# Optimization experiments

Hardware: AMD Instinct MI355X
Metric: run time of the kernel (lower is better)

## Reference

```python
import jax, jax.numpy as jnp
import numpy as np

TAPS, DIMS, SPS = 32, 2, 2
LR_W, LR_F, LR_S, LR_B = 1.0 / 2**6, 1.0 / 2**7, 0.0, 1.0 / 2**11
GRAD_MAX_W, GRAD_MAX_F = 30.0, 30.0
EPS, BETA = 1e-8, 0.0


def _const16qam():
    # commplax comm.const('16QAM', norm=True): unit-average-power 16QAM grid
    p = np.array([-3.0, -1.0, 1.0, 3.0], dtype=np.float32)
    c = (p[:, None] + 1j * p[None, :]).reshape(-1) / np.sqrt(10.0)
    return jnp.asarray(c, dtype=jnp.complex64)


def _frame(x, flen, fstep):
    # xop.frame: [L, D] -> [(L-flen)//fstep + 1, flen, D]
    n = (x.shape[0] - flen) // fstep + 1
    idx = jnp.arange(n)[:, None] * fstep + jnp.arange(flen)[None, :]
    return x[idx]


def _clip(g, gmax):
    # same math as jnp.where(|g|>gmax, g/|g|*gmax, g), but NaN-safe under AD
    ag = jnp.abs(g)
    return g * jnp.minimum(1.0, gmax / jnp.maximum(ag, 1e-30))


def _ddlms(x):
    const = _const16qam()
    u_all = _frame(x, TAPS, SPS)  # [N, taps, dims] complex64

    def step(state, u):
        w, f, s, b, fshat = state
        v = jnp.einsum('ijt,tj->i', w, u)          # mimo filter output [dims]
        k = v * f
        c = k * s
        z = c + b
        q = v * fshat + b
        # decision-directed symbol (train=False, no truth)
        d = const[jnp.argmin(jnp.abs(const[:, None] - q[None, :]), axis=0)]
        psi_hat = jnp.abs(f) / f * jnp.abs(s) / s
        e_w = (d - b) * psi_hat - v
        e_f = d - b - k
        e_s = d - b - c
        e_b = d - z
        gw = -1.0 / ((jnp.abs(u) ** 2).sum() + EPS) * e_w[:, None, None] * u.conj().T[None, ...]
        gf = -1.0 / (jnp.abs(v) ** 2 + EPS) * e_f * v.conj()
        gs = -1.0 / (jnp.abs(k) ** 2 + EPS) * e_s * k.conj()
        gb = -e_b
        gw = _clip(gw, GRAD_MAX_W)
        gf = _clip(gf, GRAD_MAX_F)
        out = (w, f, s, b)  # pre-update params are used by apply
        wn = w - LR_W * gw
        fn = f - LR_F * gf
        sn = s - LR_S * gs
        bn = b - LR_B * gb
        fshatn = BETA * fshat + (1.0 - BETA) * (fn * sn)
        return (wn, fn, sn, bn, fshatn), out

    dt = jnp.complex64
    state0 = (jnp.zeros((DIMS, DIMS, TAPS), dt),   # w0 (mimoinit='zeros')
              jnp.ones((DIMS,), dt),               # f0
              jnp.ones((DIMS,), dt),               # s0
              jnp.zeros((DIMS,), dt),              # b0
              jnp.ones((DIMS,), dt))               # fshat0
    _, (ws, fs, ss, bs) = jax.lax.scan(step, state0, u_all)
    # mimo_apply: vmap(mimo)(ws, u_all) * fs * ss + bs
    y = jnp.einsum('nijt,ntj->ni', ws, u_all) * fs * ss + bs  # [N, dims]
    return y


def setup_inputs() -> dict:
    key = jax.random.key(0)
    k1, k2 = jax.random.split(key)
    x_re = jax.random.normal(k1, (200000, 2), dtype=jnp.float32)
    x_im = jax.random.normal(k2, (200000, 2), dtype=jnp.float32)
    return {"x_re": x_re, "x_im": x_im}


def reference(x_re, x_im):
    x = jax.lax.complex(x_re, x_im)  # [2N, 2] complex64
    y = _ddlms(x)                    # [(2N-taps)//sps + 1, 2] complex64
    return jnp.stack([y.real, y.imag], axis=-1)  # [N_out, 2, 2] float32
```

## Files before the change

### kernel.cpp

```cpp
#include <hip/hip_runtime.h>

typedef unsigned u2v __attribute__((ext_vector_type(2)));

template<int CTRL>
__device__ __forceinline__ float dpp_xadd(float v) {
    int s = __builtin_amdgcn_update_dpp(0, __float_as_int(v), CTRL, 0xF, 0xF, true);
    return v + __int_as_float(s);
}

#if __has_builtin(__builtin_amdgcn_permlane16_swap)
__device__ __forceinline__ float xor16_add(float v) {
    u2v r = __builtin_amdgcn_permlane16_swap((unsigned)__float_as_int(v),
                                             (unsigned)__float_as_int(v),
                                             false, false);
    return __int_as_float((int)r.x) + __int_as_float((int)r.y);
}
#else
__device__ __forceinline__ float xor16_add(float v) {
    int s = __builtin_amdgcn_ds_swizzle(__float_as_int(v), 0x401F);
    return v + __int_as_float(s);
}
#endif

__device__ __forceinline__ float red32(float v) {
    v = dpp_xadd<0xB1>(v);
    v = dpp_xadd<0x4E>(v);
    v = dpp_xadd<0x141>(v);
    v = dpp_xadd<0x140>(v);
    v = xor16_add(v);
    return v;
}

__global__ void pre_tab(const float* __restrict__ xre,
                        const float* __restrict__ xim,
                        float4* __restrict__ tab, int ns) {
    int n = blockIdx.x * blockDim.x + threadIdx.x;
    if (n >= ns) return;
    const float* ar = xre + 4 * n;
    const float* ai = xim + 4 * n;
    float un = 0.f;
    #pragma unroll 8
    for (int k = 0; k < 64; ++k) un = fmaf(ar[k], ar[k], fmaf(ai[k], ai[k], un));
    float s = (1.0f / 64.0f) / (un + 1e-8f);
    float cr = 0.f, ci = 0.f;
    if (n + 1 < ns) {
        const float* br_ = ar + 4;
        const float* bi_ = ai + 4;
        #pragma unroll 8
        for (int k = 0; k < 64; ++k) {
            cr = fmaf(ar[k], br_[k], fmaf(ai[k], bi_[k], cr));
            ci = fmaf(ar[k], bi_[k], ci);
            ci = fmaf(-ai[k], br_[k], ci);
        }
    }
    tab[n] = make_float4(s, s * cr, s * ci, 0.f);
}

template<bool PRE>
__global__ __launch_bounds__(64, 1)
void ddlms_scan(const float* __restrict__ xre,
                const float* __restrict__ xim,
                const float4* __restrict__ tab,
                float* __restrict__ out) {
    const int l = (int)threadIdx.x;
    const int m = l & 31;
    const int half = l >> 5;

    constexpr float EPSv = 1e-8f;
    constexpr float LRW  = 1.0f / 64.0f;
    constexpr float LRF  = 1.0f / 128.0f;
    constexpr float LRB  = 1.0f / 2048.0f;
    const float B1 = 0.6324555320336759f;
    const float A1 = 0.31622776601683794f;
    const float A3 = 0.9486832980505138f;

    float wAr=0.f, wAi=0.f, wBr=0.f, wBi=0.f;
    float fr=1.f, fi=0.f, br=0.f, bi=0.f;
    float psr=1.f, psj=0.f;
    float vr=0.f, vi=0.f;
    float ewPr=0.f, ewPi=0.f, sP=0.f;

    float2* __restrict__ o2 = reinterpret_cast<float2*>(out);
    const int NS = 99985;

    auto LOADU = [&](int nn, float& a, float& b_, float& c, float& d_) {
        const float* pr = xre + 4 * nn;
        const float* pi = xim + 4 * nn;
        a = pr[m]; c = pr[m + 32]; b_ = pi[m]; d_ = pi[m + 32];
    };

    float pAr, pAi, pBr, pBi;
    float qAr, qAi, qBr, qBi;
    float rAr, rAi, rBr, rBi;
    pAr = pAi = pBr = pBi = 0.f;
    LOADU(0, qAr, qAi, qBr, qBi);
    LOADU(1, rAr, rAi, rBr, rBi);

    auto STEP = [&](int n,
        float& uPAr, float& uPAi, float& uPBr, float& uPBi,
        float& uCAr, float& uCAi, float& uCBr, float& uCBi,
        float& uNAr, float& uNAi, float& uNBr, float& uNBi) {

        {
            float gr = ewPr * uPAr; gr = fmaf( ewPi, uPAi, gr);
            float gi = ewPi * uPAr; gi = fmaf(-ewPr, uPAi, gi);
            wAr = fmaf(sP, gr, wAr); wAi = fmaf(sP, gi, wAi);
            float hr = ewPr * uPBr; hr = fmaf( ewPi, uPBi, hr);
            float hi = ewPi * uPBr; hi = fmaf(-ewPr, uPBi, hi);
            wBr = fmaf(sP, hr, wBr); wBi = fmaf(sP, hi, wBi);
        }

        float basr, basi;
        {
            float prr = wAr * uNAr; prr = fmaf(-wAi, uNAi, prr);
            prr = fmaf(wBr, uNBr, prr); prr = fmaf(-wBi, uNBi, prr);
            float pri = wAr * uNAi; pri = fmaf( wAi, uNAr, pri);
            pri = fmaf(wBr, uNBi, pri); pri = fmaf( wBi, uNBr, pri);
            basr = red32(prr); basi = red32(pri);
        }

        float sN, sCr, sCi;
        if constexpr (PRE) {
            float4 t = tab[n];
            sN = t.x; sCr = t.y; sCi = t.z;
        } else {
            float uu = uCAr * uCAr; uu = fmaf(uCAi, uCAi, uu);
            uu = fmaf(uCBr, uCBr, uu); uu = fmaf(uCBi, uCBi, uu);
            sN = LRW * __builtin_amdgcn_rcpf(red32(uu) + EPSv);
            float ccr = uCAr * uNAr; ccr = fmaf(uCAi, uNAi, ccr);
            ccr = fmaf(uCBr, uNBr, ccr); ccr = fmaf(uCBi, uNBi, ccr);
            float cci = uCAr * uNAi; cci = fmaf(-uCAi, uNAr, cci);
            cci = fmaf(uCBr, uNBi, cci); cci = fmaf(-uCBi, uNBr, cci);
            sCr = sN * red32(ccr); sCi = sN * red32(cci);
        }

        float kr = fmaf(vr, fr, -(vi * fi));
        float ki = fmaf(vr, fi,   vi * fr);
        float zr = kr + br, zi = ki + bi;
        if (m == 0) o2[2 * n + half] = make_float2(zr, zi);

        float magr = (fabsf(zr) > B1) ? A3 : A1;
        float dr   = (zr <= 0.f) ? -magr : magr;
        float magi = (fabsf(zi) > B1) ? A3 : A1;
        float di   = (zi <= 0.f) ? -magi : magi;

        float er = dr - zr, ei = di - zi;

        float v2  = fmaf(vr, vr, fmaf(vi, vi, EPSv));
        float rv  = __builtin_amdgcn_rcpf(v2);
        float gfr = fmaf(er, vr,   ei * vi)  * rv;
        float gfi = fmaf(ei, vr, -(er * vi)) * rv;
        float m2  = fmaf(gfr, gfr, gfi * gfi);
        float scf = fminf(1.f, 30.f * __builtin_amdgcn_rsqf(m2));
        float tf  = LRF * scf;

        float dbr = dr - br, dbi = di - bi;
        float ewr = fmaf(dbr, psr, -(dbi * psj)) - vr;
        float ewi = fmaf(dbr, psj,   dbi * psr)  - vi;

        float Dr = fmaf(ewr, sCr, -(ewi * sCi));
        float Di = fmaf(ewr, sCi,   ewi * sCr);
        vr = basr + Dr;
        vi = basi + Di;

        fr = fmaf(tf, gfr, fr); fi = fmaf(tf, gfi, fi);
        br = fmaf(LRB, er, br); bi = fmaf(LRB, ei, bi);

        float ff = fmaf(fr, fr, fi * fi);
        float rs = __builtin_amdgcn_rsqf(ff);
        psr = fr * rs; psj = -(fi * rs);

        ewPr = ewr; ewPi = ewi; sP = sN;

        int nn = n + 2; if (nn > NS - 1) nn = NS - 1;
        LOADU(nn, uPAr, uPAi, uPBr, uPBi);
    };

    int n = 0;
    for (int it = 0; it < 33328; ++it) {
        STEP(n,     pAr,pAi,pBr,pBi,  qAr,qAi,qBr,qBi,  rAr,rAi,rBr,rBi);
        STEP(n + 1, qAr,qAi,qBr,qBi,  rAr,rAi,rBr,rBi,  pAr,pAi,pBr,pBi);
        STEP(n + 2, rAr,rAi,rBr,rBi,  pAr,pAi,pBr,pBi,  qAr,qAi,qBr,qBi);
        n += 3;
    }
    STEP(99984, pAr,pAi,pBr,pBi, qAr,qAi,qBr,qBi, rAr,rAi,rBr,rBi);
}

extern "C" void kernel_launch(void* const* d_in, const int* in_sizes, int n_in,
                              void* d_out, int out_size, void* d_ws, size_t ws_size,
                              hipStream_t stream) {
    const float* xre = (const float*)d_in[0];
    const float* xim = (const float*)d_in[1];
    float* out = (float*)d_out;
    const int NS = 99985;

    if (ws_size >= (size_t)NS * sizeof(float4)) {
        float4* tab = (float4*)d_ws;
        pre_tab<<<(NS + 255) / 256, 256, 0, stream>>>(xre, xim, tab, NS);
        ddlms_scan<true><<<1, 64, 0, stream>>>(xre, xim, tab, out);
    } else {
        ddlms_scan<false><<<1, 64, 0, stream>>>(xre, xim, nullptr, out);
    }
}
```

Before: 23.38 ms.

## Use packed f32 complex math and deepen input/table prefetch to three steps

Rewrites the serial DD-LMS scan's complex arithmetic with inline-asm packed v_pk_mul/v_pk_fma helpers operating on float2 pairs, cutting VALU instruction count on the per-step critical path. The input ring buffer grows from three to four slots and the precomputed table entry is now prefetched three steps ahead instead of loaded in the step that uses it, hiding global memory latency. The table layout is reordered so the scale and correlation terms load as packed pairs. Hand-written asm limits compiler scheduling, and packed ops may not shorten the dependent latency chain.

```diff
diff --git a/kernel.cpp b/kernel.cpp
--- a/kernel.cpp
+++ b/kernel.cpp
@@ -1,5 +1,6 @@
 #include <hip/hip_runtime.h>
 
+typedef float f2 __attribute__((ext_vector_type(2)));
 typedef unsigned u2v __attribute__((ext_vector_type(2)));
 
 template<int CTRL>
@@ -29,6 +30,57 @@
     v = dpp_xadd<0x140>(v);
     v = xor16_add(v);
     return v;
+}
+
+
+__device__ __forceinline__ f2 cmul(f2 a, f2 b) {
+    f2 t, r;
+    asm("v_pk_mul_f32 %0, %1, %2 op_sel_hi:[0,1]" : "=v"(t) : "v"(a), "v"(b));
+    asm("v_pk_fma_f32 %0, %1, %2, %3 op_sel:[1,1,0] op_sel_hi:[1,0,1] neg_lo:[1,0,0]"
+        : "=v"(r) : "v"(a), "v"(b), "v"(t));
+    return r;
+}
+
+__device__ __forceinline__ f2 cmulc(f2 a, f2 b) {
+    f2 t, r;
+    asm("v_pk_mul_f32 %0, %1, %2 op_sel_hi:[1,0]" : "=v"(t) : "v"(a), "v"(b));
+    asm("v_pk_fma_f32 %0, %1, %2, %3 op_sel:[1,1,0] op_sel_hi:[0,1,1] neg_hi:[1,0,0]"
+        : "=v"(r) : "v"(a), "v"(b), "v"(t));
+    return r;
+}
+
+__device__ __forceinline__ f2 cfma(f2 a, f2 b, f2 acc) {
+    f2 t, r;
+    asm("v_pk_fma_f32 %0, %1, %2, %3 op_sel_hi:[0,1,1]"
+        : "=v"(t) : "v"(a), "v"(b), "v"(acc));
+    asm("v_pk_fma_f32 %0, %1, %2, %3 op_sel:[1,1,0] op_sel_hi:[1,0,1] neg_lo:[1,0,0]"
+        : "=v"(r) : "v"(a), "v"(b), "v"(t));
+    return r;
+}
+
+__device__ __forceinline__ f2 cadd(f2 a, f2 b) {
+    f2 r; asm("v_pk_add_f32 %0, %1, %2" : "=v"(r) : "v"(a), "v"(b)); return r;
+}
+__device__ __forceinline__ f2 csub(f2 a, f2 b) {
+    f2 r;
+    asm("v_pk_add_f32 %0, %1, %2 neg_lo:[0,1] neg_hi:[0,1]" : "=v"(r) : "v"(a), "v"(b));
+    return r;
+}
+__device__ __forceinline__ f2 smul(f2 s, f2 a) {
+    f2 r;
+    asm("v_pk_mul_f32 %0, %1, %2 op_sel_hi:[0,1]" : "=v"(r) : "v"(s), "v"(a));
+    return r;
+}
+__device__ __forceinline__ f2 smulconj(f2 s, f2 a) {
+    f2 r;
+    asm("v_pk_mul_f32 %0, %1, %2 op_sel_hi:[0,1] neg_hi:[0,1]" : "=v"(r) : "v"(s), "v"(a));
+    return r;
+}
+__device__ __forceinline__ f2 sfma(f2 s, f2 g, f2 w) {
+    f2 r;
+    asm("v_pk_fma_f32 %0, %1, %2, %3 op_sel_hi:[0,1,1]"
+        : "=v"(r) : "v"(s), "v"(g), "v"(w));
+    return r;
 }
 
 __global__ void pre_tab(const float* __restrict__ xre,
@@ -53,7 +105,7 @@
             ci = fmaf(-ai[k], br_[k], ci);
         }
     }
-    tab[n] = make_float4(s, s * cr, s * ci, 0.f);
+    tab[n] = make_float4(s, 0.f, s * cr, s * ci);
 }
 
 template<bool PRE>
@@ -74,116 +126,117 @@
     const float A1 = 0.31622776601683794f;
     const float A3 = 0.9486832980505138f;
 
-    float wAr=0.f, wAi=0.f, wBr=0.f, wBi=0.f;
-    float fr=1.f, fi=0.f, br=0.f, bi=0.f;
-    float psr=1.f, psj=0.f;
-    float vr=0.f, vi=0.f;
-    float ewPr=0.f, ewPi=0.f, sP=0.f;
+    f2 wA = {0.f, 0.f}, wB = {0.f, 0.f};
+    f2 ff2 = {1.f, 0.f};
+    f2 bb  = {0.f, 0.f};
+    f2 psi = {1.f, 0.f};
+    f2 vv  = {0.f, 0.f};
+    f2 ewP = {0.f, 0.f};
+    f2 sPv = {0.f, 0.f};
+    const f2 LRBD = {LRB, LRB};
 
     float2* __restrict__ o2 = reinterpret_cast<float2*>(out);
     const int NS = 99985;
 
-    auto LOADU = [&](int nn, float& a, float& b_, float& c, float& d_) {
+    auto LOADU = [&](int nn, f2& a, f2& b_) {
         const float* pr = xre + 4 * nn;
         const float* pi = xim + 4 * nn;
-        a = pr[m]; c = pr[m + 32]; b_ = pi[m]; d_ = pi[m + 32];
+        a.x = pr[m];      a.y = pi[m];
+        b_.x = pr[m + 32]; b_.y = pi[m + 32];
     };
-
-    float pAr, pAi, pBr, pBi;
-    float qAr, qAi, qBr, qBi;
-    float rAr, rAi, rBr, rBi;
-    pAr = pAi = pBr = pBi = 0.f;
-    LOADU(0, qAr, qAi, qBr, qBi);
-    LOADU(1, rAr, rAi, rBr, rBi);
+    auto LOADT = [&](int nn, float4& t) {
+        if constexpr (PRE) t = tab[nn];
+    };
+
+    f2 u0A, u0B, u1A, u1B, u2A, u2B, u3A, u3B;
+    float4 t0 = {0,0,0,0}, t1 = {0,0,0,0}, t2 = {0,0,0,0}, t3 = {0,0,0,0};
+
+    u3A = f2{0.f, 0.f}; u3B = f2{0.f, 0.f};
+    LOADU(0, u0A, u0B);
+    LOADU(1, u1A, u1B);
+    LOADU(2, u2A, u2B);
+    LOADT(0, t0); LOADT(1, t1); LOADT(2, t2);
 
     auto STEP = [&](int n,
-        float& uPAr, float& uPAi, float& uPBr, float& uPBi,
-        float& uCAr, float& uCAi, float& uCBr, float& uCBi,
-        float& uNAr, float& uNAi, float& uNBr, float& uNBi) {
+        f2& uPA, f2& uPB,
+        f2& uCA, f2& uCB,
+        f2& uNA, f2& uNB,
+        float4& tC, float4& tF) {
+
+        wA = sfma(sPv, cmulc(ewP, uPA), wA);
+        wB = sfma(sPv, cmulc(ewP, uPB), wB);
 
         {
-            float gr = ewPr * uPAr; gr = fmaf( ewPi, uPAi, gr);
-            float gi = ewPi * uPAr; gi = fmaf(-ewPr, uPAi, gi);
-            wAr = fmaf(sP, gr, wAr); wAi = fmaf(sP, gi, wAi);
-            float hr = ewPr * uPBr; hr = fmaf( ewPi, uPBi, hr);
-            float hi = ewPi * uPBr; hi = fmaf(-ewPr, uPBi, hi);
-            wBr = fmaf(sP, hr, wBr); wBi = fmaf(sP, hi, wBi);
+            int nn = n + 3; if (nn > NS - 1) nn = NS - 1;
+            LOADU(nn, uPA, uPB);
+            LOADT(nn, tF);
         }
 
-        float basr, basi;
-        {
-            float prr = wAr * uNAr; prr = fmaf(-wAi, uNAi, prr);
-            prr = fmaf(wBr, uNBr, prr); prr = fmaf(-wBi, uNBi, prr);
-            float pri = wAr * uNAi; pri = fmaf( wAi, uNAr, pri);
-            pri = fmaf(wBr, uNBi, pri); pri = fmaf( wBi, uNBr, pri);
-            basr = red32(prr); basi = red32(pri);
+        f2 acc = cmul(wA, uNA);
+        acc = cfma(wB, uNB, acc);
+        f2 bas; bas.x = red32(acc.x); bas.y = red32(acc.y);
+
+        f2 sNv, sC;
+        if constexpr (PRE) {
+            sNv = f2{tC.x, tC.y};
+            sC  = f2{tC.z, tC.w};
+        } else {
+            float uu = uCA.x * uCA.x; uu = fmaf(uCA.y, uCA.y, uu);
+            uu = fmaf(uCB.x, uCB.x, uu); uu = fmaf(uCB.y, uCB.y, uu);
+            float sN = LRW * __builtin_amdgcn_rcpf(red32(uu) + EPSv);
+            float ccr = uCA.x * uNA.x; ccr = fmaf(uCA.y, uNA.y, ccr);
+            ccr = fmaf(uCB.x, uNB.x, ccr); ccr = fmaf(uCB.y, uNB.y, ccr);
+            float cci = uCA.x * uNA.y; cci = fmaf(-uCA.y, uNA.x, cci);
+            cci = fmaf(uCB.x, uNB.y, cci); cci = fmaf(-uCB.y, uNB.x, cci);
+            sNv = f2{sN, 0.f};
+            sC  = f2{sN * red32(ccr), sN * red32(cci)};
         }
 
-        float sN, sCr, sCi;
-        if constexpr (PRE) {
-            float4 t = tab[n];
-            sN = t.x; sCr = t.y; sCi = t.z;
-        } else {
-            float uu = uCAr * uCAr; uu = fmaf(uCAi, uCAi, uu);
-            uu = fmaf(uCBr, uCBr, uu); uu = fmaf(uCBi, uCBi, uu);
-            sN = LRW * __builtin_amdgcn_rcpf(red32(uu) + EPSv);
-            float ccr = uCAr * uNAr; ccr = fmaf(uCAi, uNAi, ccr);
-            ccr = fmaf(uCBr, uNBr, ccr); ccr = fmaf(uCBi, uNBi, ccr);
-            float cci = uCAr * uNAi; cci = fmaf(-uCAi, uNAr, cci);
-            cci = fmaf(uCBr, uNBi, cci); cci = fmaf(-uCBi, uNBr, cci);
-            sCr = sN * red32(ccr); sCi = sN * red32(cci);
-        }
-
-        float kr = fmaf(vr, fr, -(vi * fi));
-        float ki = fmaf(vr, fi,   vi * fr);
-        float zr = kr + br, zi = ki + bi;
-        if (m == 0) o2[2 * n + half] = make_float2(zr, zi);
-
-        float magr = (fabsf(zr) > B1) ? A3 : A1;
-        float dr   = (zr <= 0.f) ? -magr : magr;
-        float magi = (fabsf(zi) > B1) ? A3 : A1;
-        float di   = (zi <= 0.f) ? -magi : magi;
-
-        float er = dr - zr, ei = di - zi;
-
-        float v2  = fmaf(vr, vr, fmaf(vi, vi, EPSv));
-        float rv  = __builtin_amdgcn_rcpf(v2);
-        float gfr = fmaf(er, vr,   ei * vi)  * rv;
-        float gfi = fmaf(ei, vr, -(er * vi)) * rv;
-        float m2  = fmaf(gfr, gfr, gfi * gfi);
+        f2 zz = cadd(cmul(vv, ff2), bb);
+        if (m == 0) o2[2 * n + half] = make_float2(zz.x, zz.y);
+
+        float magr = (fabsf(zz.x) > B1) ? A3 : A1;
+        float dr_  = (zz.x <= 0.f) ? -magr : magr;
+        float magi = (fabsf(zz.y) > B1) ? A3 : A1;
+        float di_  = (zz.y <= 0.f) ? -magi : magi;
+        f2 dd; dd.x = dr_; dd.y = di_;
+
+        f2 ee = csub(dd, zz);
+        f2 db = csub(dd, bb);
+
+        float v2 = fmaf(vv.x, vv.x, fmaf(vv.y, vv.y, EPSv));
+        float rv = __builtin_amdgcn_rcpf(v2);
+        f2 rvv; rvv.x = rv; rvv.y = rv;
+        f2 gf = smul(rvv, cmulc(ee, vv));
+        float m2 = fmaf(gf.x, gf.x, gf.y * gf.y);
         float scf = fminf(1.f, 30.f * __builtin_amdgcn_rsqf(m2));
-        float tf  = LRF * scf;
-
-        float dbr = dr - br, dbi = di - bi;
-        float ewr = fmaf(dbr, psr, -(dbi * psj)) - vr;
-        float ewi = fmaf(dbr, psj,   dbi * psr)  - vi;
-
-        float Dr = fmaf(ewr, sCr, -(ewi * sCi));
-        float Di = fmaf(ewr, sCi,   ewi * sCr);
-        vr = basr + Dr;
-        vi = basi + Di;
-
-        fr = fmaf(tf, gfr, fr); fi = fmaf(tf, gfi, fi);
-        br = fmaf(LRB, er, br); bi = fmaf(LRB, ei, bi);
-
-        float ff = fmaf(fr, fr, fi * fi);
-        float rs = __builtin_amdgcn_rsqf(ff);
-        psr = fr * rs; psj = -(fi * rs);
-
-        ewPr = ewr; ewPi = ewi; sP = sN;
-
-        int nn = n + 2; if (nn > NS - 1) nn = NS - 1;
-        LOADU(nn, uPAr, uPAi, uPBr, uPBi);
+        float tf = LRF * scf;
+        f2 tfv; tfv.x = tf; tfv.y = tf;
+
+        f2 ew = csub(cmul(db, psi), vv);
+
+        vv = cadd(bas, cmul(ew, sC));
+
+        ff2 = sfma(tfv, gf, ff2);
+        bb  = sfma(LRBD, ee, bb);
+
+        float ffn = fmaf(ff2.x, ff2.x, ff2.y * ff2.y);
+        float rs = __builtin_amdgcn_rsqf(ffn);
+        f2 rsv; rsv.x = rs; rsv.y = rs;
+        psi = smulconj(rsv, ff2);
+
+        ewP = ew; sPv = sNv;
     };
 
     int n = 0;
-    for (int it = 0; it < 33328; ++it) {
-        STEP(n,     pAr,pAi,pBr,pBi,  qAr,qAi,qBr,qBi,  rAr,rAi,rBr,rBi);
-        STEP(n + 1, qAr,qAi,qBr,qBi,  rAr,rAi,rBr,rBi,  pAr,pAi,pBr,pBi);
-        STEP(n + 2, rAr,rAi,rBr,rBi,  pAr,pAi,pBr,pBi,  qAr,qAi,qBr,qBi);
-        n += 3;
+    for (int it = 0; it < 24996; ++it) {
+        STEP(n+0, u3A,u3B, u0A,u0B, u1A,u1B, t0, t3);
+        STEP(n+1, u0A,u0B, u1A,u1B, u2A,u2B, t1, t0);
+        STEP(n+2, u1A,u1B, u2A,u2B, u3A,u3B, t2, t1);
+        STEP(n+3, u2A,u2B, u3A,u3B, u0A,u0B, t3, t2);
+        n += 4;
     }
-    STEP(99984, pAr,pAi,pBr,pBi, qAr,qAi,qBr,qBi, rAr,rAi,rBr,rBi);
+    STEP(99984, u3A,u3B, u0A,u0B, u1A,u1B, t0, t3);
 }
 
 extern "C" void kernel_launch(void* const* d_in, const int* in_sizes, int n_in,
```

New measurement: 25.10 ms. +7.3%, slower.

## Split serial DD-LMS scan across two wavefronts with shared-memory handoff

Applied to the files above, without the earlier changes.

The single-wavefront scan is replaced by a two-wavefront kernel. One wave runs the scalar decision, f, b and phase recursion, while the other does the tap-weight update and MIMO filter dot-product reduction. They exchange the base filter output and the scaled error through double-buffered LDS slots each step, with a __syncthreads per step. The aim is to take the weight update and cross-lane reduction off the serial critical path, at the cost of a block barrier every step.

```diff
diff --git a/kernel.cpp b/kernel.cpp
--- a/kernel.cpp
+++ b/kernel.cpp
@@ -56,16 +56,145 @@
     tab[n] = make_float4(s, s * cr, s * ci, 0.f);
 }
 
-template<bool PRE>
+#define NSTEPS 99985
+
+__global__ __launch_bounds__(128, 1)
+void ddlms_scan2(const float* __restrict__ xre,
+                 const float* __restrict__ xim,
+                 const float4* __restrict__ tab,
+                 float* __restrict__ out) {
+    const int tid = (int)threadIdx.x;
+    const int wid = tid >> 6;
+    const int l = tid & 63;
+    const int m = l & 31;
+    const int half = l >> 5;
+
+    constexpr float EPSv = 1e-8f;
+    constexpr float LRF  = 1.0f / 128.0f;
+    constexpr float LRB  = 1.0f / 2048.0f;
+    const float B1 = 0.6324555320336759f;
+    const float A1 = 0.31622776601683794f;
+    const float A3 = 0.9486832980505138f;
+
+    __shared__ float2 sh[8];
+    if (tid < 8) sh[tid] = make_float2(0.f, 0.f);
+    __syncthreads();
+
+    float2* __restrict__ o2 = reinterpret_cast<float2*>(out);
+
+    if (wid == 0) {
+        float fr = 1.f, fi = 0.f, br = 0.f, bi = 0.f, psr = 1.f, psj = 0.f;
+        float ewPr = 0.f, ewPi = 0.f, sCPr = 0.f, sCPi = 0.f;
+        float4 t0 = tab[0], t1 = tab[1], t2 = tab[2], t3;
+
+        auto W0 = [&](int n, int P, float4& tC, float4& tF) {
+            __syncthreads();
+            float2 bas = sh[2 * P + half];
+            float Dr = fmaf(ewPr, sCPr, -(ewPi * sCPi));
+            float Di = fmaf(ewPr, sCPi,   ewPi * sCPr);
+            float vr = bas.x + Dr, vi = bas.y + Di;
+            { int nn = n + 3; if (nn > NSTEPS - 1) nn = NSTEPS - 1; tF = tab[nn]; }
+
+            float kr = fmaf(vr, fr, -(vi * fi));
+            float ki = fmaf(vr, fi,   vi * fr);
+            float zr = kr + br, zi = ki + bi;
+            if (m == 0) o2[2 * n + half] = make_float2(zr, zi);
+
+            float magr = (fabsf(zr) > B1) ? A3 : A1;
+            float dr   = (zr <= 0.f) ? -magr : magr;
+            float magi = (fabsf(zi) > B1) ? A3 : A1;
+            float di   = (zi <= 0.f) ? -magi : magi;
+
+            float er = dr - zr, ei = di - zi;
+
+            float v2  = fmaf(vr, vr, fmaf(vi, vi, EPSv));
+            float rv  = __builtin_amdgcn_rcpf(v2);
+            float gfr = fmaf(er, vr,   ei * vi)  * rv;
+            float gfi = fmaf(ei, vr, -(er * vi)) * rv;
+            float m2  = fmaf(gfr, gfr, gfi * gfi);
+            float scf = fminf(1.f, 30.f * __builtin_amdgcn_rsqf(m2));
+            float tf  = LRF * scf;
+
+            float dbr = dr - br, dbi = di - bi;
+            float ewr = fmaf(dbr, psr, -(dbi * psj)) - vr;
+            float ewi = fmaf(dbr, psj,   dbi * psr)  - vi;
+
+            float ewsr = tC.x * ewr, ewsi = tC.x * ewi;
+            if (m == 0) sh[4 + 2 * P + half] = make_float2(ewsr, ewsi);
+
+            fr = fmaf(tf, gfr, fr); fi = fmaf(tf, gfi, fi);
+            br = fmaf(LRB, er, br); bi = fmaf(LRB, ei, bi);
+
+            float ff = fmaf(fr, fr, fi * fi);
+            float rs = __builtin_amdgcn_rsqf(ff);
+            psr = fr * rs; psj = -(fi * rs);
+
+            ewPr = ewr; ewPi = ewi; sCPr = tC.y; sCPi = tC.z;
+        };
+
+        int n = 0;
+        for (int it = 0; it < 24996; ++it) {
+            W0(n + 0, 0, t0, t3);
+            W0(n + 1, 1, t1, t0);
+            W0(n + 2, 0, t2, t1);
+            W0(n + 3, 1, t3, t2);
+            n += 4;
+        }
+        W0(99984, 0, t0, t3);
+    } else {
+        float wAr = 0.f, wAi = 0.f, wBr = 0.f, wBi = 0.f;
+
+        auto LOADU = [&](int nn, float& a, float& b_, float& c, float& d_) {
+            const float* pr = xre + 4 * nn;
+            const float* pi = xim + 4 * nn;
+            a = pr[m]; c = pr[m + 32]; b_ = pi[m]; d_ = pi[m + 32];
+        };
+
+        float u0Ar, u0Ai, u0Br, u0Bi, u1Ar, u1Ai, u1Br, u1Bi,
+              u2Ar, u2Ai, u2Br, u2Bi, u3Ar, u3Ai, u3Br, u3Bi;
+        u3Ar = u3Ai = u3Br = u3Bi = 0.f;
+        LOADU(0, u0Ar, u0Ai, u0Br, u0Bi);
+        LOADU(1, u1Ar, u1Ai, u1Br, u1Bi);
+        LOADU(2, u2Ar, u2Ai, u2Br, u2Bi);
+
+        auto W1 = [&](int n, int P,
+            float& uPAr, float& uPAi, float& uPBr, float& uPBi,
+            float& uNAr, float& uNAi, float& uNBr, float& uNBi) {
+            __syncthreads();
+            float2 ews = sh[4 + 2 * (1 - P) + half];
+            wAr = fmaf(ews.x, uPAr, fmaf( ews.y, uPAi, wAr));
+            wAi = fmaf(ews.y, uPAr, fmaf(-ews.x, uPAi, wAi));
+            wBr = fmaf(ews.x, uPBr, fmaf( ews.y, uPBi, wBr));
+            wBi = fmaf(ews.y, uPBr, fmaf(-ews.x, uPBi, wBi));
+            { int nn = n + 3; if (nn > NSTEPS - 1) nn = NSTEPS - 1;
+              LOADU(nn, uPAr, uPAi, uPBr, uPBi); }
+            float prr = wAr * uNAr; prr = fmaf(-wAi, uNAi, prr);
+            prr = fmaf(wBr, uNBr, prr); prr = fmaf(-wBi, uNBi, prr);
+            float pri = wAr * uNAi; pri = fmaf( wAi, uNAr, pri);
+            pri = fmaf(wBr, uNBi, pri); pri = fmaf( wBi, uNBr, pri);
+            float basr = red32(prr), basi = red32(pri);
+            if (m == 0) sh[2 * (1 - P) + half] = make_float2(basr, basi);
+        };
+
+        int n = 0;
+        for (int it = 0; it < 24996; ++it) {
+            W1(n + 0, 0, u3Ar,u3Ai,u3Br,u3Bi, u1Ar,u1Ai,u1Br,u1Bi);
+            W1(n + 1, 1, u0Ar,u0Ai,u0Br,u0Bi, u2Ar,u2Ai,u2Br,u2Bi);
+            W1(n + 2, 0, u1Ar,u1Ai,u1Br,u1Bi, u3Ar,u3Ai,u3Br,u3Bi);
+            W1(n + 3, 1, u2Ar,u2Ai,u2Br,u2Bi, u0Ar,u0Ai,u0Br,u0Bi);
+            n += 4;
+        }
+        W1(99984, 0, u3Ar,u3Ai,u3Br,u3Bi, u1Ar,u1Ai,u1Br,u1Bi);
+    }
+}
+
 __global__ __launch_bounds__(64, 1)
-void ddlms_scan(const float* __restrict__ xre,
-                const float* __restrict__ xim,
-                const float4* __restrict__ tab,
-                float* __restrict__ out) {
+void ddlms_scan_fb(const float* __restrict__ xre,
+                   const float* __restrict__ xim,
+                   float* __restrict__ out) {
     const int l = (int)threadIdx.x;
     const int m = l & 31;
     const int half = l >> 5;
-
     constexpr float EPSv = 1e-8f;
     constexpr float LRW  = 1.0f / 64.0f;
     constexpr float LRF  = 1.0f / 128.0f;
@@ -73,34 +202,23 @@
     const float B1 = 0.6324555320336759f;
     const float A1 = 0.31622776601683794f;
     const float A3 = 0.9486832980505138f;
-
     float wAr=0.f, wAi=0.f, wBr=0.f, wBi=0.f;
-    float fr=1.f, fi=0.f, br=0.f, bi=0.f;
-    float psr=1.f, psj=0.f;
-    float vr=0.f, vi=0.f;
-    float ewPr=0.f, ewPi=0.f, sP=0.f;
-
+    float fr=1.f, fi=0.f, br=0.f, bi=0.f, psr=1.f, psj=0.f;
+    float vr=0.f, vi=0.f, ewPr=0.f, ewPi=0.f, sP=0.f;
     float2* __restrict__ o2 = reinterpret_cast<float2*>(out);
-    const int NS = 99985;
-
     auto LOADU = [&](int nn, float& a, float& b_, float& c, float& d_) {
         const float* pr = xre + 4 * nn;
         const float* pi = xim + 4 * nn;
         a = pr[m]; c = pr[m + 32]; b_ = pi[m]; d_ = pi[m + 32];
     };
-
-    float pAr, pAi, pBr, pBi;
-    float qAr, qAi, qBr, qBi;
-    float rAr, rAi, rBr, rBi;
-    pAr = pAi = pBr = pBi = 0.f;
-    LOADU(0, qAr, qAi, qBr, qBi);
-    LOADU(1, rAr, rAi, rBr, rBi);
-
+    float pAr,pAi,pBr,pBi, qAr,qAi,qBr,qBi, rAr,rAi,rBr,rBi;
+    pAr=pAi=pBr=pBi=0.f;
+    LOADU(0, qAr,qAi,qBr,qBi);
+    LOADU(1, rAr,rAi,rBr,rBi);
     auto STEP = [&](int n,
         float& uPAr, float& uPAi, float& uPBr, float& uPBi,
         float& uCAr, float& uCAi, float& uCBr, float& uCBi,
         float& uNAr, float& uNAi, float& uNBr, float& uNBi) {
-
         {
             float gr = ewPr * uPAr; gr = fmaf( ewPi, uPAi, gr);
             float gi = ewPi * uPAr; gi = fmaf(-ewPr, uPAi, gi);
@@ -109,7 +227,6 @@
             float hi = ewPi * uPBr; hi = fmaf(-ewPr, uPBi, hi);
             wBr = fmaf(sP, hr, wBr); wBi = fmaf(sP, hi, wBi);
         }
-
         float basr, basi;
         {
             float prr = wAr * uNAr; prr = fmaf(-wAi, uNAi, prr);
@@ -118,34 +235,23 @@
             pri = fmaf(wBr, uNBi, pri); pri = fmaf( wBi, uNBr, pri);
             basr = red32(prr); basi = red32(pri);
         }
-
-        float sN, sCr, sCi;
-        if constexpr (PRE) {
-            float4 t = tab[n];
-            sN = t.x; sCr = t.y; sCi = t.z;
-        } else {
-            float uu = uCAr * uCAr; uu = fmaf(uCAi, uCAi, uu);
-            uu = fmaf(uCBr, uCBr, uu); uu = fmaf(uCBi, uCBi, uu);
-            sN = LRW * __builtin_amdgcn_rcpf(red32(uu) + EPSv);
-            float ccr = uCAr * uNAr; ccr = fmaf(uCAi, uNAi, ccr);
-            ccr = fmaf(uCBr, uNBr, ccr); ccr = fmaf(uCBi, uNBi, ccr);
-            float cci = uCAr * uNAi; cci = fmaf(-uCAi, uNAr, cci);
-            cci = fmaf(uCBr, uNBi, cci); cci = fmaf(-uCBi, uNBr, cci);
-            sCr = sN * red32(ccr); sCi = sN * red32(cci);
-        }
-
+        float uu = uCAr*uCAr; uu = fmaf(uCAi,uCAi,uu);
+        uu = fmaf(uCBr,uCBr,uu); uu = fmaf(uCBi,uCBi,uu);
+        float sN = LRW * __builtin_amdgcn_rcpf(red32(uu) + EPSv);
+        float ccr = uCAr*uNAr; ccr = fmaf(uCAi,uNAi,ccr);
+        ccr = fmaf(uCBr,uNBr,ccr); ccr = fmaf(uCBi,uNBi,ccr);
+        float cci = uCAr*uNAi; cci = fmaf(-uCAi,uNAr,cci);
+        cci = fmaf(uCBr,uNBi,cci); cci = fmaf(-uCBi,uNBr,cci);
+        float sCr = sN * red32(ccr), sCi = sN * red32(cci);
         float kr = fmaf(vr, fr, -(vi * fi));
         float ki = fmaf(vr, fi,   vi * fr);
         float zr = kr + br, zi = ki + bi;
         if (m == 0) o2[2 * n + half] = make_float2(zr, zi);
-
         float magr = (fabsf(zr) > B1) ? A3 : A1;
         float dr   = (zr <= 0.f) ? -magr : magr;
         float magi = (fabsf(zi) > B1) ? A3 : A1;
         float di   = (zi <= 0.f) ? -magi : magi;
-
         float er = dr - zr, ei = di - zi;
-
         float v2  = fmaf(vr, vr, fmaf(vi, vi, EPSv));
         float rv  = __builtin_amdgcn_rcpf(v2);
         float gfr = fmaf(er, vr,   ei * vi)  * rv;
@@ -153,29 +259,21 @@
         float m2  = fmaf(gfr, gfr, gfi * gfi);
         float scf = fminf(1.f, 30.f * __builtin_amdgcn_rsqf(m2));
         float tf  = LRF * scf;
-
         float dbr = dr - br, dbi = di - bi;
         float ewr = fmaf(dbr, psr, -(dbi * psj)) - vr;
         float ewi = fmaf(dbr, psj,   dbi * psr)  - vi;
-
         float Dr = fmaf(ewr, sCr, -(ewi * sCi));
         float Di = fmaf(ewr, sCi,   ewi * sCr);
-        vr = basr + Dr;
-        vi = basi + Di;
-
+        vr = basr + Dr; vi = basi + Di;
         fr = fmaf(tf, gfr, fr); fi = fmaf(tf, gfi, fi);
         br = fmaf(LRB, er, br); bi = fmaf(LRB, ei, bi);
-
         float ff = fmaf(fr, fr, fi * fi);
         float rs = __builtin_amdgcn_rsqf(ff);
         psr = fr * rs; psj = -(fi * rs);
-
         ewPr = ewr; ewPi = ewi; sP = sN;
-
-        int nn = n + 2; if (nn > NS - 1) nn = NS - 1;
+        int nn = n + 2; if (nn > NSTEPS - 1) nn = NSTEPS - 1;
         LOADU(nn, uPAr, uPAi, uPBr, uPBi);
     };
-
     int n = 0;
     for (int it = 0; it < 33328; ++it) {
         STEP(n,     pAr,pAi,pBr,pBi,  qAr,qAi,qBr,qBi,  rAr,rAi,rBr,rBi);
@@ -192,13 +290,13 @@
     const float* xre = (const float*)d_in[0];
     const float* xim = (const float*)d_in[1];
     float* out = (float*)d_out;
-    const int NS = 99985;
+    const int NS = NSTEPS;
 
     if (ws_size >= (size_t)NS * sizeof(float4)) {
         float4* tab = (float4*)d_ws;
         pre_tab<<<(NS + 255) / 256, 256, 0, stream>>>(xre, xim, tab, NS);
-        ddlms_scan<true><<<1, 64, 0, stream>>>(xre, xim, tab, out);
+        ddlms_scan2<<<1, 128, 0, stream>>>(xre, xim, tab, out);
     } else {
-        ddlms_scan<false><<<1, 64, 0, stream>>>(xre, xim, nullptr, out);
+        ddlms_scan_fb<<<1, 64, 0, stream>>>(xre, xim, out);
     }
 }
```

After: 19.63 ms. 1.19x faster.
